# Kernel tuning notes

Measured on AMD Instinct MI355X. Metric: run time of the kernel, lower is better.

## Reference

```python
import jax, jax.numpy as jnp
import numpy as np
import math

B = 1024
G = 34  # grid_dim = 17*2
C = 4
SCENT = 19


def _scent_kernel_np():
    h = w = SCENT
    mx, my = 0.5 * h, 0.5 * w
    sx, sy = h / 4.0, w / 4.0
    x = np.linspace(0.0, h, h)
    y = np.linspace(0.0, w, w)
    X, Y = np.meshgrid(x, y, indexing='ij')
    z = (1.0 / (2.0 * math.pi * sx * sy)) * np.exp(-(((X - mx) ** 2) / (2 * sx ** 2) + ((Y - my) ** 2) / (2 * sy ** 2)))
    return (z * 80.0).astype(np.float32)


def setup_inputs() -> dict:
    key = jax.random.key(0)
    k1, k2, k3, k4 = jax.random.split(key, 4)
    cell = jax.random.uniform(k1, (B, C, G, G), dtype=jnp.float32)
    food = (jax.random.uniform(k2, (B, G, G), dtype=jnp.float32) > 0.97).astype(jnp.float32)
    fc1_w = jax.random.normal(k3, (64, 12), dtype=jnp.float32) * (1.0 / np.sqrt(12))
    fc1_b = jnp.zeros((64,), dtype=jnp.float32)
    fc2_w = jax.random.normal(k4, (4, 64), dtype=jnp.float32) * (1.0 / np.sqrt(64))
    fc2_b = jnp.zeros((4,), dtype=jnp.float32)
    scent_kernel = jnp.asarray(_scent_kernel_np())
    return {"cell": cell, "food": food, "fc1_w": fc1_w, "fc1_b": fc1_b,
            "fc2_w": fc2_w, "fc2_b": fc2_b, "scent_kernel": scent_kernel, "steps": 32}


def _conv(x, w, pad, groups):
    # x: [B, Cin, H, W], w: [Cout, Cin/groups, kh, kw]; cross-correlation like torch
    return jax.lax.conv_general_dilated(
        x, w, window_strides=(1, 1), padding=[(pad, pad), (pad, pad)],
        feature_group_count=groups, dimension_numbers=('NCHW', 'OIHW', 'NCHW'))


def _maxpool3(x):
    # 3x3 max pool, stride 1, pad 1 (pad value -inf, matching torch MaxPool2d semantics)
    return jax.lax.reduce_window(x, -jnp.inf, jax.lax.max, (1, 1, 3, 3), (1, 1, 1, 1),
                                 [(0, 0), (0, 0), (1, 1), (1, 1)])


def _forward(cell, food, fc1_w, fc1_b, fc2_w, fc2_b, scent_kernel, steps):
    dx = jnp.outer(jnp.array([1., 2., 1.], jnp.float32), jnp.array([-1., 0., 1.], jnp.float32)) / 8.0
    dy = dx.T
    kdx = jnp.tile(dx[None, None], (4, 1, 1, 1))  # depthwise, groups=4
    kdy = jnp.tile(dy[None, None], (4, 1, 1, 1))

    # perceive_scent: 19x19 gaussian conv, padding 9
    scent = _conv(food[:, None], scent_kernel[None, None], 9, 1)[:, 0]  # [B,G,G]

    def step(cell, _):
        cell = cell.at[:, 3].set(scent)
        # current living count per batch (cells in channel 0 above 0.8)
        cl = jnp.sum((cell[:, 0] > 0.8).astype(jnp.float32), axis=(1, 2))
        pre_mask = _maxpool3(cell[:, 0:1]) > 0.1  # [B,1,G,G]
        # perception: x, sobel-x, sobel-y -> 12 channels
        y1 = _conv(cell, kdx, 1, 4)
        y2 = _conv(cell, kdy, 1, 4)
        y = jnp.concatenate([cell, y1, y2], axis=1)  # [B,12,G,G]
        # tiny MLP per pixel (torch transposes dims 1<->3; linear over channels is equivalent)
        h = jax.nn.relu(jnp.einsum('bchw,oc->bohw', y, fc1_w) + fc1_b[None, :, None, None])
        upd = jnp.einsum('bchw,oc->bohw', h, fc2_w) + fc2_b[None, :, None, None]
        x = cell + upd
        post_mask = _maxpool3(x[:, 0:1]) > 0.1
        x = x * (pre_mask & post_mask).astype(x.dtype)
        x = jnp.clip(x, -10.0, 10.0)
        x = x.at[:, 0].set(jnp.clip(x[:, 0], 0.0, 1.0))
        # keep_k_largest: threshold = cl-th smallest (ascending sort index == cl); keep strictly greater
        flat = x[:, 0].reshape(B, -1)  # [B, G*G]
        srt = jnp.sort(flat, axis=1)
        kth = jnp.take_along_axis(srt, cl.astype(jnp.int32)[:, None], axis=1)  # [B,1] (gather clamps OOB)
        flat = jnp.where(flat > kth, flat, 0.0)
        x = x.at[:, 0].set(flat.reshape(B, G, G))
        return x, None

    cell, _ = jax.lax.scan(jax.checkpoint(step), cell, None, length=steps)
    total_pixel_val = cell[:, 0:1].sum(axis=(1, 2, 3))
    living_count = jnp.sum((cell[:, 0:1] > 0.1).astype(jnp.float32), axis=(1, 2, 3))
    return cell, food, total_pixel_val, living_count


def reference(cell, food, fc1_w, fc1_b, fc2_w, fc2_b, scent_kernel, steps):
    return _forward(cell, food, fc1_w, fc1_b, fc2_w, fc2_b, scent_kernel, steps)
```

## Files before the change

kernel.cpp:

```cpp
#include <hip/hip_runtime.h>
#include <stdint.h>

#define GD    34
#define GP    36
#define NPIX  1156
#define NT    256
#define NB    1024
#define TPR   7
#define TUSED 238

#define SCAN_PASS(KK) do {                                                         \
    if (wid == 0) {                                                                \
      const int base2 = lane << 4;                                                 \
      int c16[16]; int csum = 0;                                                   \
      _Pragma("unroll")                                                            \
      for (int j = 0; j < 16; ++j) { c16[j] = hist[base2+j]; hist[base2+j] = 0; csum += c16[j]; } \
      int inc = csum;                                                              \
      _Pragma("unroll")                                                            \
      for (int off2 = 1; off2 < 64; off2 <<= 1) { int vv = __shfl_up(inc, off2); if (lane >= off2) inc += vv; } \
      const int excl = inc - csum;                                                 \
      if ((KK) >= excl && (KK) < inc) {                                            \
        int rem = (KK) - excl; int cum = 0;                                        \
        _Pragma("unroll")                                                          \
        for (int j = 0; j < 16; ++j) {                                             \
          if (rem >= cum && rem < cum + c16[j]) { sel_bin = base2 + j; sel_rem = rem - cum; } \
          cum += c16[j];                                                           \
        }                                                                          \
      }                                                                            \
    }                                                                              \
  } while (0)

#define SCRN 4904

__global__ __launch_bounds__(NT) __attribute__((amdgpu_waves_per_eu(4, 4)))
void ca_kernel(const float* __restrict__ cell_in,
               const float* __restrict__ food_in,
               const float* __restrict__ fc1_w,
               const float* __restrict__ fc1_b,
               const float* __restrict__ fc2_w,
               const float* __restrict__ fc2_b,
               const float* __restrict__ sk_g,
               const int*   __restrict__ steps_p,
               float* __restrict__ out)
{
  __shared__ float cbuf[3][GP*GP];
  __shared__ float scratch[SCRN];
  __shared__ int   icl[2][4];
  __shared__ int   inzaz[4];
  __shared__ int   sel_bin, sel_rem;
  __shared__ float fsum[4];
  __shared__ int   lcnt[4];

  float* x0buf = scratch;
  float* x1s   = scratch + 1296;
  float* x2s   = scratch + 2452;
  int*   premi = (int*)(scratch + 3608);
  int*   hist  = (int*)(scratch + 1296);

  const int tid  = threadIdx.x;
  const int b    = blockIdx.x;
  const int lane = tid & 63;
  const int wid  = tid >> 6;
  const int nsteps = steps_p[0];

  const bool tval = (tid < TUSED);
  const int  trow = tval ? (tid / TPR) : 0;
  const int  c0   = tval ? ((tid % TPR) * 5) : 0;
  const int  nval = tval ? ((c0 <= 29) ? 5 : 4) : 0;
  const int  pb0  = tval ? ((trow+1)*GP + c0 + 1) : 37;
  const int  p0   = trow*GD + c0;

  for (int idx = tid; idx < 3*GP*GP; idx += NT) (&cbuf[0][0])[idx] = 0.f;
  for (int idx = tid; idx < SCRN;    idx += NT) scratch[idx] = 0.f;
  __syncthreads();

  float v3k[5];
  int cnt0 = 0;
#pragma unroll
  for (int j = 0; j < 5; ++j) {
    v3k[j] = 0.f;
    if (j < nval) {
      int p = p0 + j;
      const float* gi = cell_in + (size_t)b*4*NPIX + p;
      float v0 = gi[0], v1 = gi[NPIX], v2 = gi[2*NPIX], v3 = gi[3*NPIX];
      cbuf[0][pb0+j] = v0; cbuf[1][pb0+j] = v1; cbuf[2][pb0+j] = v2;
      v3k[j] = v3;
      cnt0 += (v0 > 0.8f) ? 1 : 0;
      scratch[(trow+9)*52 + (c0+j+9)] = food_in[(size_t)b*NPIX + p];
    }
  }
#pragma unroll
  for (int off = 32; off; off >>= 1) cnt0 += __shfl_down(cnt0, off);
  if (lane == 0) icl[0][wid] = cnt0;
  __syncthreads();

  float scent[5];
#pragma unroll
  for (int j = 0; j < 5; ++j) {
    float ssum = 0.f;
    if (j < nval) {
      for (int dr = 0; dr < 19; ++dr) {
        const float* frow = scratch + (trow+dr)*52 + (c0+j);
        const float* krow = sk_g + dr*19;
#pragma unroll
        for (int dc = 0; dc < 19; ++dc) ssum = fmaf(frow[dc], krow[dc], ssum);
      }
    }
    scent[j] = ssum;
  }
  __syncthreads();
  for (int idx = tid; idx < SCRN; idx += NT) scratch[idx] = 0.f;
  __syncthreads();
#pragma unroll
  for (int j = 0; j < 5; ++j) if (j < nval) x0buf[pb0+j] = scent[j];
  __syncthreads();
  float sxs[5], sys[5];
#pragma unroll
  for (int j = 0; j < 5; ++j) {
    const int bb = (j < nval) ? (pb0 + j) : pb0;
    float t00=x0buf[bb-GP-1], t01=x0buf[bb-GP], t02=x0buf[bb-GP+1];
    float t10=x0buf[bb-1],                      t12=x0buf[bb+1];
    float t20=x0buf[bb+GP-1], t21=x0buf[bb+GP], t22=x0buf[bb+GP+1];
    sxs[j] = ((t02 - t00) + 2.f*(t12 - t10) + (t22 - t20)) * 0.125f;
    sys[j] = ((t20 - t00) + 2.f*(t21 - t01) + (t22 - t02)) * 0.125f;
  }

  const float b2r0 = fc2_b[0], b2r1 = fc2_b[1], b2r2 = fc2_b[2], b2r3 = fc2_b[3];

  for (int s = 0; s < nsteps; ++s) {
    __syncthreads();
    float cm[7];
#pragma unroll
    for (int jc = 0; jc < 7; ++jc) {
      cm[jc] = 0.f;
      if (jc < nval + 2) {
        const int a = pb0 - 1 + jc;
        cm[jc] = fmaxf(fmaxf(cbuf[0][a-GP], cbuf[0][a]), cbuf[0][a+GP]);
      }
    }
    unsigned pm = 0;
#pragma unroll
    for (int j = 0; j < 5; ++j) {
      if (j < nval) {
        bool t = fmaxf(fmaxf(cm[j], cm[j+1]), cm[j+2]) > 0.1f;
        premi[pb0+j] = t ? 1 : 0;
        if (t) pm |= (1u << j);
      }
    }
    __syncthreads();
    int co[7];
#pragma unroll
    for (int jc = 0; jc < 7; ++jc) {
      co[jc] = 0;
      if (jc < nval + 2) {
        const int a = pb0 - 1 + jc;
        co[jc] = premi[a-GP] | premi[a] | premi[a+GP];
      }
    }
#pragma unroll
    for (int j = 0; j < 5; ++j) {
      int acti = (j < nval) ? (co[j] | co[j+1] | co[j+2]) : 0;
      if (__any(acti)) {
        const int bb = (j < nval) ? (pb0 + j) : pb0;
        float y0,y1,y2,y4,y5,y6,y8,y9,y10;
        {
          const float* cb = cbuf[0];
          float t00=cb[bb-GP-1], t01=cb[bb-GP], t02=cb[bb-GP+1];
          float t10=cb[bb-1],    t11=cb[bb],    t12=cb[bb+1];
          float t20=cb[bb+GP-1], t21=cb[bb+GP], t22=cb[bb+GP+1];
          y0 = t11;
          y4 = ((t02 - t00) + 2.f*(t12 - t10) + (t22 - t20)) * 0.125f;
          y8 = ((t20 - t00) + 2.f*(t21 - t01) + (t22 - t02)) * 0.125f;
        }
        {
          const float* cb = cbuf[1];
          float t00=cb[bb-GP-1], t01=cb[bb-GP], t02=cb[bb-GP+1];
          float t10=cb[bb-1],    t11=cb[bb],    t12=cb[bb+1];
          float t20=cb[bb+GP-1], t21=cb[bb+GP], t22=cb[bb+GP+1];
          y1 = t11;
          y5 = ((t02 - t00) + 2.f*(t12 - t10) + (t22 - t20)) * 0.125f;
          y9 = ((t20 - t00) + 2.f*(t21 - t01) + (t22 - t02)) * 0.125f;
        }
        {
          const float* cb = cbuf[2];
          float t00=cb[bb-GP-1], t01=cb[bb-GP], t02=cb[bb-GP+1];
          float t10=cb[bb-1],    t11=cb[bb],    t12=cb[bb+1];
          float t20=cb[bb+GP-1], t21=cb[bb+GP], t22=cb[bb+GP+1];
          y2 = t11;
          y6 = ((t02 - t00) + 2.f*(t12 - t10) + (t22 - t20)) * 0.125f;
          y10= ((t20 - t00) + 2.f*(t21 - t01) + (t22 - t02)) * 0.125f;
        }
        const float y3 = scent[j], y7 = sxs[j], y11 = sys[j];
        float u0 = b2r0, u1 = b2r1, u2 = b2r2, u3 = b2r3;
        for (int o = 0; o < 64; ++o) {
          const float* wr = fc1_w + o*12;
          float t = fc1_b[o];
          t = fmaf(y0, wr[0], t);  t = fmaf(y1, wr[1], t);
          t = fmaf(y2, wr[2], t);  t = fmaf(y3, wr[3], t);
          t = fmaf(y4, wr[4], t);  t = fmaf(y5, wr[5], t);
          t = fmaf(y6, wr[6], t);  t = fmaf(y7, wr[7], t);
          t = fmaf(y8, wr[8], t);  t = fmaf(y9, wr[9], t);
          t = fmaf(y10, wr[10], t); t = fmaf(y11, wr[11], t);
          t = fmaxf(t, 0.f);
          u0 = fmaf(t, fc2_w[o],     u0);
          u1 = fmaf(t, fc2_w[64+o],  u1);
          u2 = fmaf(t, fc2_w[128+o], u2);
          u3 = fmaf(t, fc2_w[192+o], u3);
        }
        v3k[j] = y3 + u3;
        if (j < nval) {
          x0buf[bb]    = y0 + u0;
          x1s[p0 + j]  = y1 + u1;
          x2s[p0 + j]  = y2 + u2;
        }
      }
    }
    __syncthreads();
    unsigned pq = 0;
    float midv[5];
#pragma unroll
    for (int j = 0; j < 5; ++j) midv[j] = 0.f;
    if (pm) {
      float dm[7];
#pragma unroll
      for (int jc = 0; jc < 7; ++jc) {
        dm[jc] = 0.f;
        if (jc < nval + 2) {
          const int a = pb0 - 1 + jc;
          float u = x0buf[a-GP], m = x0buf[a], d = x0buf[a+GP];
          dm[jc] = fmaxf(fmaxf(u, m), d);
          if (jc >= 1 && jc <= 5) midv[jc-1] = m;
        }
      }
#pragma unroll
      for (int j = 0; j < 5; ++j)
        if (fmaxf(fmaxf(dm[j], dm[j+1]), dm[j+2]) > 0.1f) pq |= (1u << j);
    }
    int packed = 0;
    float v0s[5];
#pragma unroll
    for (int j = 0; j < 5; ++j) {
      v0s[j] = 0.f;
      if (j < nval) {
        bool alive = ((pm >> j) & 1u) && ((pq >> j) & 1u);
        float v0 = 0.f, v1 = 0.f, v2 = 0.f, v3 = 0.f;
        if (alive) {
          v0 = fminf(fmaxf(midv[j],      0.f),  1.f);
          v1 = fminf(fmaxf(x1s[p0+j], -10.f), 10.f);
          v2 = fminf(fmaxf(x2s[p0+j], -10.f), 10.f);
          v3 = fminf(fmaxf(v3k[j],    -10.f), 10.f);
        }
        cbuf[1][pb0+j] = v1; cbuf[2][pb0+j] = v2; v3k[j] = v3;
        v0s[j] = v0;
        int zer = (v0 == 0.f) ? 1 : 0;
        int azf = (zer && v1 == 0.f && v2 == 0.f && v3 == 0.f) ? 1 : 0;
        packed += zer + (azf << 16);
      }
    }
#pragma unroll
    for (int off = 32; off; off >>= 1) packed += __shfl_down(packed, off);
    if (lane == 0) inzaz[wid] = packed;
    __syncthreads();
    const int t01 = inzaz[0]+inzaz[1]+inzaz[2]+inzaz[3];
    const int nz = t01 & 0xffff, az = t01 >> 16;
    const int cl = icl[s&1][0]+icl[s&1][1]+icl[s&1][2]+icl[s&1][3];
    const int k  = (cl < NPIX) ? cl : (NPIX-1);
    float kth = 0.f;
    if (k >= nz) {
      hist[tid] = 0; hist[tid+256] = 0; hist[tid+512] = 0; hist[tid+768] = 0;
      __syncthreads();
      const int k2 = k - nz;
#pragma unroll
      for (int j = 0; j < 5; ++j) {
        unsigned u = __float_as_uint(v0s[j]);
        if (j < nval && u != 0u) atomicAdd(&hist[u >> 20], 1);
      }
      __syncthreads();
      SCAN_PASS(k2);
      __syncthreads();
      const int bin1 = sel_bin; const int kr2 = sel_rem;
#pragma unroll
      for (int j = 0; j < 5; ++j) {
        unsigned u = __float_as_uint(v0s[j]);
        if (j < nval && u != 0u && (u >> 20) == (unsigned)bin1)
          atomicAdd(&hist[(u >> 10) & 1023u], 1);
      }
      __syncthreads();
      SCAN_PASS(kr2);
      __syncthreads();
      const int bin2 = sel_bin; const int kr3 = sel_rem;
      const unsigned pref2 = (((unsigned)bin1) << 10) | (unsigned)bin2;
#pragma unroll
      for (int j = 0; j < 5; ++j) {
        unsigned u = __float_as_uint(v0s[j]);
        if (j < nval && u != 0u && (u >> 10) == pref2)
          atomicAdd(&hist[u & 1023u], 1);
      }
      __syncthreads();
      SCAN_PASS(kr3);
      __syncthreads();
      kth = __uint_as_float((((unsigned)bin1) << 20) | (((unsigned)bin2) << 10) | (unsigned)sel_bin);
    }
    int cnt = 0;
#pragma unroll
    for (int j = 0; j < 5; ++j) {
      if (j < nval) {
        float w0 = (v0s[j] > kth) ? v0s[j] : 0.f;
        cbuf[0][pb0+j] = w0;
        cnt += (w0 > 0.8f) ? 1 : 0;
      }
    }
#pragma unroll
    for (int off = 32; off; off >>= 1) cnt += __shfl_down(cnt, off);
    if (lane == 0) icl[(s+1)&1][wid] = cnt;
    if (az == NPIX) break;
  }

  const size_t CELL_N = (size_t)4*NPIX*NB;
  const size_t FOOD_N = (size_t)NPIX*NB;
  float tp = 0.f; int lcv = 0;
#pragma unroll
  for (int j = 0; j < 5; ++j) {
    if (j < nval) {
      const int p = p0 + j;
      float c0v = cbuf[0][pb0+j], c1 = cbuf[1][pb0+j], c2 = cbuf[2][pb0+j];
      size_t go = (size_t)b*4*NPIX + p;
      out[go]          = c0v;
      out[go +   NPIX] = c1;
      out[go + 2*NPIX] = c2;
      out[go + 3*NPIX] = v3k[j];
      out[CELL_N + (size_t)b*NPIX + p] = food_in[(size_t)b*NPIX + p];
      tp += c0v;
      lcv += (c0v > 0.1f) ? 1 : 0;
    }
  }
#pragma unroll
  for (int off = 32; off; off >>= 1) { tp += __shfl_down(tp, off); lcv += __shfl_down(lcv, off); }
  if (lane == 0) { fsum[wid] = tp; lcnt[wid] = lcv; }
  __syncthreads();
  if (tid == 0) {
    out[CELL_N + FOOD_N + b]      = fsum[0]+fsum[1]+fsum[2]+fsum[3];
    out[CELL_N + FOOD_N + NB + b] = (float)(lcnt[0]+lcnt[1]+lcnt[2]+lcnt[3]);
  }
}

extern "C" void kernel_launch(void* const* d_in, const int* in_sizes, int n_in,
                              void* d_out, int out_size, void* d_ws, size_t ws_size,
                              hipStream_t stream) {
  const float* cell  = (const float*)d_in[0];
  const float* food  = (const float*)d_in[1];
  const float* fc1w  = (const float*)d_in[2];
  const float* fc1b  = (const float*)d_in[3];
  const float* fc2w  = (const float*)d_in[4];
  const float* fc2b  = (const float*)d_in[5];
  const float* sk    = (const float*)d_in[6];
  const int*   steps = (const int*)d_in[7];
  float* out = (float*)d_out;
  ca_kernel<<<NB, NT, 0, stream>>>(cell, food, fc1w, fc1b, fc2w, fc2b, sk, steps, out);
}
```

Baseline: 266.1 us.

## Pad LDS rows, keep channel updates in registers, register-block scent conv

Changes the padded row stride of the shared cell buffers from 36 to 39 and the food scratch stride from 52 to 57, which is meant to reduce LDS bank conflicts. Channel 1/2 updates now stay in registers instead of round-tripping through shared scratch, which also shrinks the scratch allocation. Channel 0 stencil values are reused from the registers loaded for the pre-life maxpool. The 19x19 scent convolution is register-blocked so each kernel weight serves five outputs from one loaded row window. In exchange, register pressure rises under the fixed 4-waves-per-EU bound.

Result: faster. 236.9 us (-11.0%).

```diff
diff --git a/kernel.cpp b/kernel.cpp
--- a/kernel.cpp
+++ b/kernel.cpp
@@ -2,12 +2,16 @@
 #include <stdint.h>
 
 #define GD    34
-#define GP    36
+#define RS    39
+#define NROW  36
+#define CBN   (NROW*RS)
 #define NPIX  1156
 #define NT    256
 #define NB    1024
 #define TPR   7
 #define TUSED 238
+#define FS    57
+#define SCRN  2960
 
 #define SCAN_PASS(KK) do {                                                         \
     if (wid == 0) {                                                                \
@@ -30,8 +34,6 @@
     }                                                                              \
   } while (0)
 
-#define SCRN 4904
-
 __global__ __launch_bounds__(NT) __attribute__((amdgpu_waves_per_eu(4, 4)))
 void ca_kernel(const float* __restrict__ cell_in,
                const float* __restrict__ food_in,
@@ -43,7 +45,7 @@
                const int*   __restrict__ steps_p,
                float* __restrict__ out)
 {
-  __shared__ float cbuf[3][GP*GP];
+  __shared__ float cbuf[3][CBN];
   __shared__ float scratch[SCRN];
   __shared__ int   icl[2][4];
   __shared__ int   inzaz[4];
@@ -52,10 +54,8 @@
   __shared__ int   lcnt[4];
 
   float* x0buf = scratch;
-  float* x1s   = scratch + 1296;
-  float* x2s   = scratch + 2452;
-  int*   premi = (int*)(scratch + 3608);
-  int*   hist  = (int*)(scratch + 1296);
+  int*   premi = (int*)(scratch + 1404);
+  int*   hist  = (int*)scratch;
 
   const int tid  = threadIdx.x;
   const int b    = blockIdx.x;
@@ -67,18 +67,18 @@
   const int  trow = tval ? (tid / TPR) : 0;
   const int  c0   = tval ? ((tid % TPR) * 5) : 0;
   const int  nval = tval ? ((c0 <= 29) ? 5 : 4) : 0;
-  const int  pb0  = tval ? ((trow+1)*GP + c0 + 1) : 37;
+  const int  pb0  = tval ? ((trow+1)*RS + c0 + 1) : (RS+1);
   const int  p0   = trow*GD + c0;
 
-  for (int idx = tid; idx < 3*GP*GP; idx += NT) (&cbuf[0][0])[idx] = 0.f;
-  for (int idx = tid; idx < SCRN;    idx += NT) scratch[idx] = 0.f;
-  __syncthreads();
-
-  float v3k[5];
+  for (int idx = tid; idx < 3*CBN; idx += NT) (&cbuf[0][0])[idx] = 0.f;
+  for (int idx = tid; idx < SCRN;  idx += NT) scratch[idx] = 0.f;
+  __syncthreads();
+
+  float v3k[5], v1k[5], v2k[5];
   int cnt0 = 0;
 #pragma unroll
   for (int j = 0; j < 5; ++j) {
-    v3k[j] = 0.f;
+    v3k[j] = 0.f; v1k[j] = 0.f; v2k[j] = 0.f;
     if (j < nval) {
       int p = p0 + j;
       const float* gi = cell_in + (size_t)b*4*NPIX + p;
@@ -86,7 +86,7 @@
       cbuf[0][pb0+j] = v0; cbuf[1][pb0+j] = v1; cbuf[2][pb0+j] = v2;
       v3k[j] = v3;
       cnt0 += (v0 > 0.8f) ? 1 : 0;
-      scratch[(trow+9)*52 + (c0+j+9)] = food_in[(size_t)b*NPIX + p];
+      scratch[(trow+9)*FS + (c0+j+9)] = food_in[(size_t)b*NPIX + p];
     }
   }
 #pragma unroll
@@ -94,19 +94,22 @@
   if (lane == 0) icl[0][wid] = cnt0;
   __syncthreads();
 
-  float scent[5];
-#pragma unroll
-  for (int j = 0; j < 5; ++j) {
-    float ssum = 0.f;
-    if (j < nval) {
-      for (int dr = 0; dr < 19; ++dr) {
-        const float* frow = scratch + (trow+dr)*52 + (c0+j);
-        const float* krow = sk_g + dr*19;
-#pragma unroll
-        for (int dc = 0; dc < 19; ++dc) ssum = fmaf(frow[dc], krow[dc], ssum);
-      }
-    }
-    scent[j] = ssum;
+  float scent[5] = {0.f, 0.f, 0.f, 0.f, 0.f};
+  for (int dr = 0; dr < 19; ++dr) {
+    const float* frow = scratch + (trow+dr)*FS + c0;
+    float f[23];
+#pragma unroll
+    for (int q = 0; q < 23; ++q) f[q] = frow[q];
+    const float* krow = sk_g + dr*19;
+#pragma unroll
+    for (int dc = 0; dc < 19; ++dc) {
+      const float kv = krow[dc];
+      scent[0] = fmaf(f[dc+0], kv, scent[0]);
+      scent[1] = fmaf(f[dc+1], kv, scent[1]);
+      scent[2] = fmaf(f[dc+2], kv, scent[2]);
+      scent[3] = fmaf(f[dc+3], kv, scent[3]);
+      scent[4] = fmaf(f[dc+4], kv, scent[4]);
+    }
   }
   __syncthreads();
   for (int idx = tid; idx < SCRN; idx += NT) scratch[idx] = 0.f;
@@ -118,9 +121,9 @@
 #pragma unroll
   for (int j = 0; j < 5; ++j) {
     const int bb = (j < nval) ? (pb0 + j) : pb0;
-    float t00=x0buf[bb-GP-1], t01=x0buf[bb-GP], t02=x0buf[bb-GP+1];
+    float t00=x0buf[bb-RS-1], t01=x0buf[bb-RS], t02=x0buf[bb-RS+1];
     float t10=x0buf[bb-1],                      t12=x0buf[bb+1];
-    float t20=x0buf[bb+GP-1], t21=x0buf[bb+GP], t22=x0buf[bb+GP+1];
+    float t20=x0buf[bb+RS-1], t21=x0buf[bb+RS], t22=x0buf[bb+RS+1];
     sxs[j] = ((t02 - t00) + 2.f*(t12 - t10) + (t22 - t20)) * 0.125f;
     sys[j] = ((t20 - t00) + 2.f*(t21 - t01) + (t22 - t02)) * 0.125f;
   }
@@ -129,13 +132,14 @@
 
   for (int s = 0; s < nsteps; ++s) {
     __syncthreads();
-    float cm[7];
+    float r0[7], r1[7], r2[7], cm[7];
 #pragma unroll
     for (int jc = 0; jc < 7; ++jc) {
-      cm[jc] = 0.f;
+      r0[jc] = 0.f; r1[jc] = 0.f; r2[jc] = 0.f; cm[jc] = 0.f;
       if (jc < nval + 2) {
         const int a = pb0 - 1 + jc;
-        cm[jc] = fmaxf(fmaxf(cbuf[0][a-GP], cbuf[0][a]), cbuf[0][a+GP]);
+        r0[jc] = cbuf[0][a-RS]; r1[jc] = cbuf[0][a]; r2[jc] = cbuf[0][a+RS];
+        cm[jc] = fmaxf(fmaxf(r0[jc], r1[jc]), r2[jc]);
       }
     }
     unsigned pm = 0;
@@ -154,38 +158,34 @@
       co[jc] = 0;
       if (jc < nval + 2) {
         const int a = pb0 - 1 + jc;
-        co[jc] = premi[a-GP] | premi[a] | premi[a+GP];
+        co[jc] = premi[a-RS] | premi[a] | premi[a+RS];
       }
     }
 #pragma unroll
     for (int j = 0; j < 5; ++j) {
       int acti = (j < nval) ? (co[j] | co[j+1] | co[j+2]) : 0;
       if (__any(acti)) {
-        const int bb = (j < nval) ? (pb0 + j) : pb0;
+        const int bb = pb0 + j;
         float y0,y1,y2,y4,y5,y6,y8,y9,y10;
         {
-          const float* cb = cbuf[0];
-          float t00=cb[bb-GP-1], t01=cb[bb-GP], t02=cb[bb-GP+1];
-          float t10=cb[bb-1],    t11=cb[bb],    t12=cb[bb+1];
-          float t20=cb[bb+GP-1], t21=cb[bb+GP], t22=cb[bb+GP+1];
-          y0 = t11;
-          y4 = ((t02 - t00) + 2.f*(t12 - t10) + (t22 - t20)) * 0.125f;
-          y8 = ((t20 - t00) + 2.f*(t21 - t01) + (t22 - t02)) * 0.125f;
+          y0 = r1[j+1];
+          y4 = ((r0[j+2] - r0[j]) + 2.f*(r1[j+2] - r1[j]) + (r2[j+2] - r2[j])) * 0.125f;
+          y8 = ((r2[j] - r0[j]) + 2.f*(r2[j+1] - r0[j+1]) + (r2[j+2] - r0[j+2])) * 0.125f;
         }
         {
           const float* cb = cbuf[1];
-          float t00=cb[bb-GP-1], t01=cb[bb-GP], t02=cb[bb-GP+1];
+          float t00=cb[bb-RS-1], t01=cb[bb-RS], t02=cb[bb-RS+1];
           float t10=cb[bb-1],    t11=cb[bb],    t12=cb[bb+1];
-          float t20=cb[bb+GP-1], t21=cb[bb+GP], t22=cb[bb+GP+1];
+          float t20=cb[bb+RS-1], t21=cb[bb+RS], t22=cb[bb+RS+1];
           y1 = t11;
           y5 = ((t02 - t00) + 2.f*(t12 - t10) + (t22 - t20)) * 0.125f;
           y9 = ((t20 - t00) + 2.f*(t21 - t01) + (t22 - t02)) * 0.125f;
         }
         {
           const float* cb = cbuf[2];
-          float t00=cb[bb-GP-1], t01=cb[bb-GP], t02=cb[bb-GP+1];
+          float t00=cb[bb-RS-1], t01=cb[bb-RS], t02=cb[bb-RS+1];
           float t10=cb[bb-1],    t11=cb[bb],    t12=cb[bb+1];
-          float t20=cb[bb+GP-1], t21=cb[bb+GP], t22=cb[bb+GP+1];
+          float t20=cb[bb+RS-1], t21=cb[bb+RS], t22=cb[bb+RS+1];
           y2 = t11;
           y6 = ((t02 - t00) + 2.f*(t12 - t10) + (t22 - t20)) * 0.125f;
           y10= ((t20 - t00) + 2.f*(t21 - t01) + (t22 - t02)) * 0.125f;
@@ -209,9 +209,9 @@
         }
         v3k[j] = y3 + u3;
         if (j < nval) {
-          x0buf[bb]    = y0 + u0;
-          x1s[p0 + j]  = y1 + u1;
-          x2s[p0 + j]  = y2 + u2;
+          x0buf[bb]  = y0 + u0;
+          v1k[j]     = y1 + u1;
+          v2k[j]     = y2 + u2;
         }
       }
     }
@@ -227,7 +227,7 @@
         dm[jc] = 0.f;
         if (jc < nval + 2) {
           const int a = pb0 - 1 + jc;
-          float u = x0buf[a-GP], m = x0buf[a], d = x0buf[a+GP];
+          float u = x0buf[a-RS], m = x0buf[a], d = x0buf[a+RS];
           dm[jc] = fmaxf(fmaxf(u, m), d);
           if (jc >= 1 && jc <= 5) midv[jc-1] = m;
         }
@@ -245,10 +245,10 @@
         bool alive = ((pm >> j) & 1u) && ((pq >> j) & 1u);
         float v0 = 0.f, v1 = 0.f, v2 = 0.f, v3 = 0.f;
         if (alive) {
-          v0 = fminf(fmaxf(midv[j],      0.f),  1.f);
-          v1 = fminf(fmaxf(x1s[p0+j], -10.f), 10.f);
-          v2 = fminf(fmaxf(x2s[p0+j], -10.f), 10.f);
-          v3 = fminf(fmaxf(v3k[j],    -10.f), 10.f);
+          v0 = fminf(fmaxf(midv[j],   0.f),  1.f);
+          v1 = fminf(fmaxf(v1k[j],  -10.f), 10.f);
+          v2 = fminf(fmaxf(v2k[j],  -10.f), 10.f);
+          v3 = fminf(fmaxf(v3k[j],  -10.f), 10.f);
         }
         cbuf[1][pb0+j] = v1; cbuf[2][pb0+j] = v2; v3k[j] = v3;
         v0s[j] = v0;
```
